# Kernel optimization log

Hardware: AMD Instinct MI355X
Metric: run time of the kernel (lower is better)

The kernel has to match this reference:

```python
import jax, jax.numpy as jnp
import numpy as np

HEADS = 16
DIM_HEAD = 64
SCALE = DIM_HEAD ** -0.5


def setup_inputs() -> dict:
    key = jax.random.key(0)
    k1, k2, k3, k4 = jax.random.split(key, 4)
    b, n, dim = 2, 2048, 1024
    inner = HEADS * DIM_HEAD  # 1024
    x = jax.random.normal(k1, (b, n, dim), dtype=jnp.float32)
    # binary keep-mask (multiplicative, as in the original module)
    seq_mask = (jax.random.uniform(k2, (b, n)) < 0.9).astype(jnp.float32)
    # weights stored [in, out] (transpose of torch Linear layout)
    w_qkv = jax.random.normal(k3, (dim, inner * 3), dtype=jnp.float32) * (dim ** -0.5)
    w_out = jax.random.normal(k4, (inner, dim), dtype=jnp.float32) * (inner ** -0.5)
    return {"x": x, "seq_mask": seq_mask, "w_qkv": w_qkv, "w_out": w_out}


def reference(x, seq_mask, w_qkv, w_out):
    b, n, dim = x.shape
    qkv = x @ w_qkv                                   # [b, n, 3*inner]
    q, k, v = jnp.split(qkv, 3, axis=-1)
    split_heads = lambda t: t.reshape(b, n, HEADS, DIM_HEAD).transpose(0, 2, 1, 3)
    q, k, v = split_heads(q), split_heads(k), split_heads(v)  # [b, h, n, d]
    dots = jnp.einsum('bhid,bhjd->bhij', q, k) * SCALE        # [b, h, n, n]
    # multiplicative mask, broadcast over heads and query index i; mask depends on key index j
    dots = dots * seq_mask[:, None, None, :]
    attn = jax.nn.softmax(dots, axis=-1)
    out = jnp.einsum('bhij,bhjd->bhid', attn, v)              # [b, h, n, d]
    out = out.transpose(0, 2, 1, 3).reshape(b, n, HEADS * DIM_HEAD)
    return out @ w_out                                        # dropout p=0 -> identity
```

## Files before the change

kernel.cpp:

```cpp
#include <hip/hip_runtime.h>
#include <hip/hip_bf16.h>

using bf16 = __hip_bfloat16;
typedef __attribute__((ext_vector_type(8))) short short8;
typedef __attribute__((ext_vector_type(4))) float floatx4;

#define MFMA_BF16(a, b, c) __builtin_amdgcn_mfma_f32_16x16x32_bf16((a), (b), (c), 0, 0, 0)

__device__ __forceinline__ void gload_lds16(const bf16* g, bf16* l) {
  __builtin_amdgcn_global_load_lds((__attribute__((address_space(1))) void*)g,
                                   (__attribute__((address_space(3))) void*)l,
                                   16, 0, 0);
}

__device__ __forceinline__ unsigned short bfbits(float f) {
  bf16 b = __float2bfloat16(f);
  return *reinterpret_cast<unsigned short*>(&b);
}

__global__ __launch_bounds__(256)
void probemask_k(const void* __restrict__ msrc, bf16* __restrict__ dst,
                 int* __restrict__ flag) {
  __shared__ int any;
  const int tid = threadIdx.x;
  if (tid == 0) any = 0;
  __syncthreads();
  const unsigned* mw = (const unsigned*)msrc;
  int bad = 0;
#pragma unroll
  for (int i = 0; i < 4; i++) {
    unsigned w = mw[tid * 4 + i];
    if (w != 0u && w != 0x3F800000u) bad = 1;
  }
  if (bad) atomicOr(&any, 1);
  __syncthreads();
  const int isbf = any;
  if (tid == 0) flag[0] = isbf;
  if (isbf) {
#pragma unroll
    for (int i = 0; i < 2; i++)
      ((int4*)dst)[tid * 2 + i] = ((const int4*)msrc)[tid * 2 + i];
  } else {
#pragma unroll
    for (int i = 0; i < 4; i++) {
      float4 v = ((const float4*)msrc)[tid * 4 + i];
      int o = tid * 16 + i * 4;
      dst[o + 0] = __float2bfloat16(v.x);
      dst[o + 1] = __float2bfloat16(v.y);
      dst[o + 2] = __float2bfloat16(v.z);
      dst[o + 3] = __float2bfloat16(v.w);
    }
  }
}

__global__ __launch_bounds__(256)
void cvt_k(const void* __restrict__ src, bf16* __restrict__ dst, int n,
           const int* __restrict__ flag) {
  if (*flag) return;
  int i = (blockIdx.x * 256 + threadIdx.x) * 4;
  if (i >= n) return;
  float4 v = ((const float4*)src)[i >> 2];
  dst[i + 0] = __float2bfloat16(v.x);
  dst[i + 1] = __float2bfloat16(v.y);
  dst[i + 2] = __float2bfloat16(v.z);
  dst[i + 3] = __float2bfloat16(v.w);
}

__global__ __launch_bounds__(256)
void transpose2_k(const void* __restrict__ in0, bf16* __restrict__ out0,
                  const void* __restrict__ in1, bf16* __restrict__ out1,
                  const int* __restrict__ flag) {
  __shared__ bf16 tile[32][33];
  const int isbf = *flag;
  constexpr int R = 1024;
  const void* in;
  bf16* out;
  int C, bx;
  if (blockIdx.x < 96) { in = in0; out = out0; C = 3072; bx = blockIdx.x * 32; }
  else                 { in = in1; out = out1; C = 1024; bx = (blockIdx.x - 96) * 32; }
  int by = blockIdx.y * 32;
  int tx = threadIdx.x & 31, ty = threadIdx.x >> 5;
#pragma unroll
  for (int i = 0; i < 4; i++) {
    size_t idx = (size_t)(by + ty + i * 8) * C + bx + tx;
    tile[ty + i * 8][tx] =
        isbf ? ((const bf16*)in)[idx] : __float2bfloat16(((const float*)in)[idx]);
  }
  __syncthreads();
#pragma unroll
  for (int i = 0; i < 4; i++)
    out[(size_t)(bx + ty + i * 8) * R + by + tx] = tile[tx][ty + i * 8];
}

template <int MODE>
__global__ __launch_bounds__(256, 2)
void gemm_k(const bf16* __restrict__ A, const bf16* __restrict__ Aalt,
            const bf16* __restrict__ Bt,
            bf16* __restrict__ Qo, bf16* __restrict__ Ko, bf16* __restrict__ Vo,
            void* __restrict__ Co, const bf16* __restrict__ Mk,
            const int* __restrict__ flag) {
  constexpr int K = 1024;
  __shared__ __align__(16) bf16 As[128 * 32];
  __shared__ __align__(16) bf16 Bs[128 * 32];

  const int tid = threadIdx.x;
  const int lane = tid & 63;
  const int wv = tid >> 6;
  const int wm = wv & 1, wn = wv >> 1;
  const int l15 = lane & 15, quad = lane >> 4;

  const int bm = blockIdx.y * 128;
  const int bn = blockIdx.x * 128;

  const int sml = tid >> 2;
  const int sg = (tid & 3) ^ ((sml >> 1) & 3);

  const bf16* Ab = (MODE == 0 && *flag) ? Aalt : A;

  floatx4 acc[4][4] = {};

  for (int k0 = 0; k0 < K; k0 += 32) {
    __syncthreads();
    const bf16 *a0, *a1;
    if (MODE == 0) {
      a0 = Ab + (size_t)(bm + sml) * K + k0 + sg * 8;
      a1 = a0 + (size_t)64 * K;
    } else {
      const int b_idx = bm >> 11;
      const int h = k0 >> 6;
      const int d = (k0 & 63) + sg * 8;
      const int nn = bm & 2047;
      const bf16* base = Ab + (size_t)(b_idx * 16 + h) * 131072 + d;
      a0 = base + (size_t)(nn + sml) * 64;
      a1 = base + (size_t)(nn + 64 + sml) * 64;
    }
    gload_lds16(a0, &As[tid * 8]);
    gload_lds16(a1, &As[2048 + tid * 8]);
    const bf16* b0 = Bt + (size_t)(bn + sml) * K + k0 + sg * 8;
    gload_lds16(b0, &Bs[tid * 8]);
    gload_lds16(b0 + (size_t)64 * K, &Bs[2048 + tid * 8]);
    __syncthreads();

    short8 af[4], bfr[4];
#pragma unroll
    for (int mi = 0; mi < 4; mi++) {
      int m = wm * 64 + mi * 16 + l15;
      af[mi] = *(const short8*)&As[m * 32 + ((quad ^ ((m >> 1) & 3)) * 8)];
    }
#pragma unroll
    for (int ni = 0; ni < 4; ni++) {
      int n = wn * 64 + ni * 16 + l15;
      bfr[ni] = *(const short8*)&Bs[n * 32 + ((quad ^ ((n >> 1) & 3)) * 8)];
    }
#pragma unroll
    for (int mi = 0; mi < 4; mi++)
#pragma unroll
      for (int ni = 0; ni < 4; ni++)
        acc[mi][ni] = MFMA_BF16(af[mi], bfr[ni], acc[mi][ni]);
  }

  const int isbf = (MODE == 1) ? *flag : 0;

#pragma unroll
  for (int mi = 0; mi < 4; mi++) {
    const int row0 = bm + wm * 64 + mi * 16 + quad * 4;
#pragma unroll
    for (int ni = 0; ni < 4; ni++) {
      const int col = bn + wn * 64 + ni * 16 + l15;
      if (MODE == 0) {
        const int sec = col >> 10;
        const int cc = col & 1023;
        const int h = cc >> 6, d = cc & 63;
        const int b_idx = row0 >> 11;
        const int nn0 = row0 & 2047;
        if (sec == 0) {
          bf16* dst = Qo + (size_t)(b_idx * 16 + h) * 131072 + (size_t)nn0 * 64 + d;
#pragma unroll
          for (int r = 0; r < 4; r++) dst[r * 64] = __float2bfloat16(acc[mi][ni][r]);
        } else if (sec == 1) {
          const bf16* mrow = Mk + (size_t)b_idx * 2048 + nn0;
          bf16* dst = Ko + (size_t)(b_idx * 16 + h) * 131072 + (size_t)nn0 * 64 + d;
#pragma unroll
          for (int r = 0; r < 4; r++)
            dst[r * 64] = __float2bfloat16(acc[mi][ni][r] * 0.125f *
                                           __bfloat162float(mrow[r]));
        } else {
          bf16* dst = Vo + (size_t)(b_idx * 16 + h) * 131072 + (size_t)d * 2048 + nn0;
#pragma unroll
          for (int r = 0; r < 4; r++) dst[r] = __float2bfloat16(acc[mi][ni][r]);
        }
      } else {
        if (isbf) {
          bf16* C2 = (bf16*)Co;
#pragma unroll
          for (int r = 0; r < 4; r++)
            C2[(size_t)(row0 + r) * 1024 + col] = __float2bfloat16(acc[mi][ni][r]);
        } else {
          float* C2 = (float*)Co;
#pragma unroll
          for (int r = 0; r < 4; r++)
            C2[(size_t)(row0 + r) * 1024 + col] = acc[mi][ni][r];
        }
      }
    }
  }
}

__global__ __launch_bounds__(256, 4)
void flash_k(const bf16* __restrict__ Q, const bf16* __restrict__ K,
             const bf16* __restrict__ VT, bf16* __restrict__ O) {
  __shared__ __align__(16) bf16 Ks[2][4096];
  __shared__ __align__(16) bf16 Vs[2][4096];
  __shared__ __align__(16) bf16 Ps[4096];

  const int tid = threadIdx.x;
  const int lane = tid & 63;
  const int w = tid >> 6;
  const int l15 = lane & 15, quad = lane >> 4;
  const int sw7 = l15 & 7;

  const int qt = blockIdx.x & 31;
  const int hl = blockIdx.x >> 5;

  const bf16* Qh = Q + (size_t)hl * 131072;
  const bf16* Kh = K + (size_t)hl * 131072;
  const bf16* Vh = VT + (size_t)hl * 131072;
  bf16* Oh = O + (size_t)hl * 131072;

  const int qrow = qt * 64 + w * 16;
  short8 qf[2];
#pragma unroll
  for (int kk = 0; kk < 2; kk++)
    qf[kk] = *(const short8*)&Qh[(size_t)(qrow + l15) * 64 + kk * 32 + quad * 8];

  floatx4 o_acc[4] = {};
  float rsum = 0.f;

  bf16* Psw = Ps + w * 1024;

  const int sjj = tid >> 3;
  const int sgp = (tid & 7) ^ (sjj & 7);

  gload_lds16(&Kh[(size_t)sjj * 64 + sgp * 8], &Ks[0][tid * 8]);
  gload_lds16(&Kh[(size_t)(32 + sjj) * 64 + sgp * 8], &Ks[0][2048 + tid * 8]);
  gload_lds16(&Vh[(size_t)sjj * 2048 + sgp * 8], &Vs[0][tid * 8]);
  gload_lds16(&Vh[(size_t)(32 + sjj) * 2048 + sgp * 8], &Vs[0][2048 + tid * 8]);

  for (int it = 0; it < 32; ++it) {
    const int b = it & 1;
    __syncthreads();
    if (it < 31) {
      const int j1 = (it + 1) * 64;
      gload_lds16(&Kh[(size_t)(j1 + sjj) * 64 + sgp * 8], &Ks[b ^ 1][tid * 8]);
      gload_lds16(&Kh[(size_t)(j1 + 32 + sjj) * 64 + sgp * 8], &Ks[b ^ 1][2048 + tid * 8]);
      gload_lds16(&Vh[(size_t)sjj * 2048 + j1 + sgp * 8], &Vs[b ^ 1][tid * 8]);
      gload_lds16(&Vh[(size_t)(32 + sjj) * 2048 + j1 + sgp * 8], &Vs[b ^ 1][2048 + tid * 8]);
    }

    floatx4 s[4] = {};
#pragma unroll
    for (int nj = 0; nj < 4; nj++) {
      const int jj = nj * 16 + l15;
#pragma unroll
      for (int kk = 0; kk < 2; kk++) {
        const int gk = kk * 4 + quad;
        short8 kf = *(const short8*)&Ks[b][jj * 64 + ((gk ^ (jj & 7)) * 8)];
        s[nj] = MFMA_BF16(kf, qf[kk], s[nj]);
      }
    }

    float rs = 0.f;
#pragma unroll
    for (int nj = 0; nj < 4; nj++)
#pragma unroll
      for (int r = 0; r < 4; r++) {
        const float p = __expf(s[nj][r]);
        s[nj][r] = p;
        rs += p;
      }
    rs += __shfl_xor(rs, 16, 64);
    rs += __shfl_xor(rs, 32, 64);
    rsum += rs;

#pragma unroll
    for (int nj = 0; nj < 4; nj++) {
      ushort4 u;
      u.x = bfbits(s[nj][0]);
      u.y = bfbits(s[nj][1]);
      u.z = bfbits(s[nj][2]);
      u.w = bfbits(s[nj][3]);
      const int G = nj * 2 + (quad >> 1), h = quad & 1;
      *(ushort4*)&Psw[l15 * 64 + ((G ^ sw7) * 8) + h * 4] = u;
    }
    __builtin_amdgcn_wave_barrier();

    short8 pf[2];
#pragma unroll
    for (int kk = 0; kk < 2; kk++)
      pf[kk] = *(const short8*)&Psw[l15 * 64 + (((kk * 4 + quad) ^ sw7) * 8)];

#pragma unroll
    for (int ni = 0; ni < 4; ni++) {
      const int dd = ni * 16 + l15;
#pragma unroll
      for (int kk = 0; kk < 2; kk++) {
        const int gk = kk * 4 + quad;
        short8 vf = *(const short8*)&Vs[b][dd * 64 + ((gk ^ (dd & 7)) * 8)];
        o_acc[ni] = MFMA_BF16(pf[kk], vf, o_acc[ni]);
      }
    }
  }

  float rinv[4];
#pragma unroll
  for (int r = 0; r < 4; r++)
    rinv[r] = 1.f / __shfl(rsum, quad * 4 + r, 64);
#pragma unroll
  for (int ni = 0; ni < 4; ni++) {
    const int d = ni * 16 + l15;
#pragma unroll
    for (int r = 0; r < 4; r++) {
      const int row = qrow + quad * 4 + r;
      Oh[(size_t)row * 64 + d] = __float2bfloat16(o_acc[ni][r] * rinv[r]);
    }
  }
}

extern "C" void kernel_launch(void* const* d_in, const int* in_sizes, int n_in,
                              void* d_out, int out_size, void* d_ws, size_t ws_size,
                              hipStream_t stream) {
  const void* x     = d_in[0];
  const void* mask  = d_in[1];
  const void* w_qkv = d_in[2];
  const void* w_out = d_in[3];

  bf16* ws    = (bf16*)d_ws;
  bf16* xb    = ws;
  bf16* AO    = ws;
  bf16* wqkvT = ws + 4194304;
  bf16* woutT = wqkvT + 3145728;
  bf16* Qb    = woutT + 1048576;
  bf16* Kb    = Qb + 4194304;
  bf16* maskb = Kb + 4194304;
  int*  flag  = (int*)(maskb + 4096);
  bf16* VT    = (bf16*)d_out;

  probemask_k<<<1, 256, 0, stream>>>(mask, maskb, flag);
  cvt_k<<<4096, 256, 0, stream>>>(x, xb, 4194304, flag);
  transpose2_k<<<dim3(128, 32), 256, 0, stream>>>(w_qkv, wqkvT, w_out, woutT, flag);
  gemm_k<0><<<dim3(24, 32), 256, 0, stream>>>(xb, (const bf16*)x, wqkvT, Qb, Kb, VT,
                                              nullptr, maskb, flag);
  flash_k<<<1024, 256, 0, stream>>>(Qb, Kb, VT, AO);
  gemm_k<1><<<dim3(8, 32), 256, 0, stream>>>(AO, nullptr, woutT, nullptr, nullptr,
                                             nullptr, d_out, nullptr, flag);
}
```

Measured before the change: 202.0 us.

## Switch flash attention to 32x32 MFMA tiles, exp2 softmax, token-major output

The attention kernel now uses 32x32x16 bf16 MFMA with 32 query rows per wave and 128 per block, doubling K/V reuse per LDS load and halving the grid. The softmax uses the hardware exp2 with log2(e) folded into the K scaling in the QKV GEMM epilogue, which replaces the natural-exp call. Attention output is written directly in [b, n, h*d] layout, so the output projection GEMM reads it with plain row-major addressing. Occupancy drops (launch bounds 2 instead of 4) and the P scratch buffer doubles, which trades latency hiding for larger tiles.

```diff
diff --git a/kernel.cpp b/kernel.cpp
--- a/kernel.cpp
+++ b/kernel.cpp
@@ -4,8 +4,10 @@
 using bf16 = __hip_bfloat16;
 typedef __attribute__((ext_vector_type(8))) short short8;
 typedef __attribute__((ext_vector_type(4))) float floatx4;
+typedef __attribute__((ext_vector_type(16))) float floatx16;
 
 #define MFMA_BF16(a, b, c) __builtin_amdgcn_mfma_f32_16x16x32_bf16((a), (b), (c), 0, 0, 0)
+#define MFMA32(a, b, c) __builtin_amdgcn_mfma_f32_32x32x16_bf16((a), (b), (c), 0, 0, 0)
 
 __device__ __forceinline__ void gload_lds16(const bf16* g, bf16* l) {
   __builtin_amdgcn_global_load_lds((__attribute__((address_space(1))) void*)g,
@@ -17,6 +19,10 @@
   bf16 b = __float2bfloat16(f);
   return *reinterpret_cast<unsigned short*>(&b);
 }
+
+__device__ __forceinline__ int swz32(int r) { return (r & 7) ^ ((r >> 3) & 3); }
+
+#define KSCALE 0.18033688011112042f
 
 __global__ __launch_bounds__(256)
 void probemask_k(const void* __restrict__ msrc, bf16* __restrict__ dst,
@@ -115,27 +121,16 @@
   const int sml = tid >> 2;
   const int sg = (tid & 3) ^ ((sml >> 1) & 3);
 
-  const bf16* Ab = (MODE == 0 && *flag) ? Aalt : A;
+  const int isbf = *flag;
+  const bf16* Ab = (MODE == 0 && isbf) ? Aalt : A;
 
   floatx4 acc[4][4] = {};
 
   for (int k0 = 0; k0 < K; k0 += 32) {
     __syncthreads();
-    const bf16 *a0, *a1;
-    if (MODE == 0) {
-      a0 = Ab + (size_t)(bm + sml) * K + k0 + sg * 8;
-      a1 = a0 + (size_t)64 * K;
-    } else {
-      const int b_idx = bm >> 11;
-      const int h = k0 >> 6;
-      const int d = (k0 & 63) + sg * 8;
-      const int nn = bm & 2047;
-      const bf16* base = Ab + (size_t)(b_idx * 16 + h) * 131072 + d;
-      a0 = base + (size_t)(nn + sml) * 64;
-      a1 = base + (size_t)(nn + 64 + sml) * 64;
-    }
+    const bf16* a0 = Ab + (size_t)(bm + sml) * K + k0 + sg * 8;
     gload_lds16(a0, &As[tid * 8]);
-    gload_lds16(a1, &As[2048 + tid * 8]);
+    gload_lds16(a0 + (size_t)64 * K, &As[2048 + tid * 8]);
     const bf16* b0 = Bt + (size_t)(bn + sml) * K + k0 + sg * 8;
     gload_lds16(b0, &Bs[tid * 8]);
     gload_lds16(b0 + (size_t)64 * K, &Bs[2048 + tid * 8]);
@@ -158,8 +153,6 @@
       for (int ni = 0; ni < 4; ni++)
         acc[mi][ni] = MFMA_BF16(af[mi], bfr[ni], acc[mi][ni]);
   }
-
-  const int isbf = (MODE == 1) ? *flag : 0;
 
 #pragma unroll
   for (int mi = 0; mi < 4; mi++) {
@@ -182,7 +175,7 @@
           bf16* dst = Ko + (size_t)(b_idx * 16 + h) * 131072 + (size_t)nn0 * 64 + d;
 #pragma unroll
           for (int r = 0; r < 4; r++)
-            dst[r * 64] = __float2bfloat16(acc[mi][ni][r] * 0.125f *
+            dst[r * 64] = __float2bfloat16(acc[mi][ni][r] * KSCALE *
                                            __bfloat162float(mrow[r]));
         } else {
           bf16* dst = Vo + (size_t)(b_idx * 16 + h) * 131072 + (size_t)d * 2048 + nn0;
@@ -206,40 +199,43 @@
   }
 }
 
-__global__ __launch_bounds__(256, 4)
+__global__ __launch_bounds__(256, 2)
 void flash_k(const bf16* __restrict__ Q, const bf16* __restrict__ K,
-             const bf16* __restrict__ VT, bf16* __restrict__ O) {
+             const bf16* __restrict__ VT, bf16* __restrict__ AO) {
   __shared__ __align__(16) bf16 Ks[2][4096];
   __shared__ __align__(16) bf16 Vs[2][4096];
-  __shared__ __align__(16) bf16 Ps[4096];
+  __shared__ __align__(16) bf16 Ps[8192];
 
   const int tid = threadIdx.x;
   const int lane = tid & 63;
   const int w = tid >> 6;
-  const int l15 = lane & 15, quad = lane >> 4;
-  const int sw7 = l15 & 7;
-
-  const int qt = blockIdx.x & 31;
-  const int hl = blockIdx.x >> 5;
+  const int l31 = lane & 31;
+  const int l5h = lane >> 5;
+  const int sw = swz32(l31);
+
+  const int qt = blockIdx.x & 15;
+  const int hl = blockIdx.x >> 4;
+  const int b_idx = hl >> 4, h = hl & 15;
 
   const bf16* Qh = Q + (size_t)hl * 131072;
   const bf16* Kh = K + (size_t)hl * 131072;
   const bf16* Vh = VT + (size_t)hl * 131072;
-  bf16* Oh = O + (size_t)hl * 131072;
-
-  const int qrow = qt * 64 + w * 16;
-  short8 qf[2];
-#pragma unroll
-  for (int kk = 0; kk < 2; kk++)
-    qf[kk] = *(const short8*)&Qh[(size_t)(qrow + l15) * 64 + kk * 32 + quad * 8];
-
-  floatx4 o_acc[4] = {};
+
+  const int qbase = qt * 128 + w * 32;
+  const int qrow = qbase + l31;
+
+  short8 qf[4];
+#pragma unroll
+  for (int c = 0; c < 4; c++)
+    qf[c] = *(const short8*)&Qh[(size_t)qrow * 64 + c * 16 + l5h * 8];
+
+  floatx16 o_acc[2] = {};
   float rsum = 0.f;
 
-  bf16* Psw = Ps + w * 1024;
+  bf16* Psw = Ps + w * 2048;
 
   const int sjj = tid >> 3;
-  const int sgp = (tid & 7) ^ (sjj & 7);
+  const int sgp = (tid & 7) ^ swz32(sjj);
 
   gload_lds16(&Kh[(size_t)sjj * 64 + sgp * 8], &Ks[0][tid * 8]);
   gload_lds16(&Kh[(size_t)(32 + sjj) * 64 + sgp * 8], &Ks[0][2048 + tid * 8]);
@@ -257,73 +253,76 @@
       gload_lds16(&Vh[(size_t)(32 + sjj) * 2048 + j1 + sgp * 8], &Vs[b ^ 1][2048 + tid * 8]);
     }
 
-    floatx4 s[4] = {};
-#pragma unroll
-    for (int nj = 0; nj < 4; nj++) {
-      const int jj = nj * 16 + l15;
-#pragma unroll
-      for (int kk = 0; kk < 2; kk++) {
-        const int gk = kk * 4 + quad;
-        short8 kf = *(const short8*)&Ks[b][jj * 64 + ((gk ^ (jj & 7)) * 8)];
-        s[nj] = MFMA_BF16(kf, qf[kk], s[nj]);
+    floatx16 s[2] = {};
+#pragma unroll
+    for (int kt = 0; kt < 2; kt++) {
+      const int key = kt * 32 + l31;
+#pragma unroll
+      for (int c = 0; c < 4; c++) {
+        const int g = c * 2 + l5h;
+        short8 kf = *(const short8*)&Ks[b][key * 64 + ((g ^ sw) * 8)];
+        s[kt] = MFMA32(kf, qf[c], s[kt]);
       }
     }
 
     float rs = 0.f;
 #pragma unroll
-    for (int nj = 0; nj < 4; nj++)
-#pragma unroll
-      for (int r = 0; r < 4; r++) {
-        const float p = __expf(s[nj][r]);
-        s[nj][r] = p;
+    for (int kt = 0; kt < 2; kt++)
+#pragma unroll
+      for (int r = 0; r < 16; r++) {
+        const float p = __builtin_amdgcn_exp2f(s[kt][r]);
+        s[kt][r] = p;
         rs += p;
       }
-    rs += __shfl_xor(rs, 16, 64);
     rs += __shfl_xor(rs, 32, 64);
     rsum += rs;
 
 #pragma unroll
-    for (int nj = 0; nj < 4; nj++) {
+    for (int kt = 0; kt < 2; kt++)
+#pragma unroll
+      for (int rg = 0; rg < 4; rg++) {
+        ushort4 u;
+        u.x = bfbits(s[kt][rg * 4 + 0]);
+        u.y = bfbits(s[kt][rg * 4 + 1]);
+        u.z = bfbits(s[kt][rg * 4 + 2]);
+        u.w = bfbits(s[kt][rg * 4 + 3]);
+        const int g = kt * 4 + rg;
+        *(ushort4*)&Psw[l31 * 64 + ((g ^ sw) * 8) + l5h * 4] = u;
+      }
+    __builtin_amdgcn_wave_barrier();
+
+    short8 pf[4];
+#pragma unroll
+    for (int c = 0; c < 4; c++) {
+      const int g = c * 2 + l5h;
+      pf[c] = *(const short8*)&Psw[l31 * 64 + ((g ^ sw) * 8)];
+    }
+
+#pragma unroll
+    for (int dt = 0; dt < 2; dt++) {
+      const int d = dt * 32 + l31;
+#pragma unroll
+      for (int c = 0; c < 4; c++) {
+        const int g = c * 2 + l5h;
+        short8 vf = *(const short8*)&Vs[b][d * 64 + ((g ^ sw) * 8)];
+        o_acc[dt] = MFMA32(vf, pf[c], o_acc[dt]);
+      }
+    }
+  }
+
+  const float rinv = 1.f / rsum;
+  bf16* orow = AO + (size_t)(b_idx * 2048 + qbase + l31) * 1024 + h * 64;
+#pragma unroll
+  for (int dt = 0; dt < 2; dt++)
+#pragma unroll
+    for (int rg = 0; rg < 4; rg++) {
       ushort4 u;
-      u.x = bfbits(s[nj][0]);
-      u.y = bfbits(s[nj][1]);
-      u.z = bfbits(s[nj][2]);
-      u.w = bfbits(s[nj][3]);
-      const int G = nj * 2 + (quad >> 1), h = quad & 1;
-      *(ushort4*)&Psw[l15 * 64 + ((G ^ sw7) * 8) + h * 4] = u;
-    }
-    __builtin_amdgcn_wave_barrier();
-
-    short8 pf[2];
-#pragma unroll
-    for (int kk = 0; kk < 2; kk++)
-      pf[kk] = *(const short8*)&Psw[l15 * 64 + (((kk * 4 + quad) ^ sw7) * 8)];
-
-#pragma unroll
-    for (int ni = 0; ni < 4; ni++) {
-      const int dd = ni * 16 + l15;
-#pragma unroll
-      for (int kk = 0; kk < 2; kk++) {
-        const int gk = kk * 4 + quad;
-        short8 vf = *(const short8*)&Vs[b][dd * 64 + ((gk ^ (dd & 7)) * 8)];
-        o_acc[ni] = MFMA_BF16(pf[kk], vf, o_acc[ni]);
-      }
-    }
-  }
-
-  float rinv[4];
-#pragma unroll
-  for (int r = 0; r < 4; r++)
-    rinv[r] = 1.f / __shfl(rsum, quad * 4 + r, 64);
-#pragma unroll
-  for (int ni = 0; ni < 4; ni++) {
-    const int d = ni * 16 + l15;
-#pragma unroll
-    for (int r = 0; r < 4; r++) {
-      const int row = qrow + quad * 4 + r;
-      Oh[(size_t)row * 64 + d] = __float2bfloat16(o_acc[ni][r] * rinv[r]);
-    }
-  }
+      u.x = bfbits(o_acc[dt][rg * 4 + 0] * rinv);
+      u.y = bfbits(o_acc[dt][rg * 4 + 1] * rinv);
+      u.z = bfbits(o_acc[dt][rg * 4 + 2] * rinv);
+      u.w = bfbits(o_acc[dt][rg * 4 + 3] * rinv);
+      *(ushort4*)&orow[dt * 32 + rg * 8 + l5h * 4] = u;
+    }
 }
 
 extern "C" void kernel_launch(void* const* d_in, const int* in_sizes, int n_in,
@@ -350,7 +349,7 @@
   transpose2_k<<<dim3(128, 32), 256, 0, stream>>>(w_qkv, wqkvT, w_out, woutT, flag);
   gemm_k<0><<<dim3(24, 32), 256, 0, stream>>>(xb, (const bf16*)x, wqkvT, Qb, Kb, VT,
                                               nullptr, maskb, flag);
-  flash_k<<<1024, 256, 0, stream>>>(Qb, Kb, VT, AO);
+  flash_k<<<512, 256, 0, stream>>>(Qb, Kb, VT, AO);
   gemm_k<1><<<dim3(8, 32), 256, 0, stream>>>(AO, nullptr, woutT, nullptr, nullptr,
                                              nullptr, d_out, nullptr, flag);
 }
```

Result: faster. 193.4 us (-4.2%).
